# Kernel tuning notes

Hardware: AMD Instinct MI355X
Metric: run time of the kernel (lower is better)

The kernel has to match this reference:

```python
import jax, jax.numpy as jnp
import numpy as np

D = 1024
HEADS = 16
HEAD_DIM = D // HEADS
B = 4
L = 1024


def setup_inputs() -> dict:
    key = jax.random.key(0)
    kq, kk, kv, kw, kb = jax.random.split(key, 5)
    Q = jax.random.normal(kq, (B, L, D), dtype=jnp.float32)
    K = jax.random.normal(kk, (B, L, D), dtype=jnp.float32)
    V = jax.random.normal(kv, (B, L, D), dtype=jnp.float32)
    # Output projection H: torch nn.Linear(D, D) -> weight (D, D), bias (D,)
    lim = 1.0 / np.sqrt(D)
    W_H = jax.random.uniform(kw, (D, D), minval=-lim, maxval=lim, dtype=jnp.float32)
    b_H = jax.random.uniform(kb, (D,), minval=-lim, maxval=lim, dtype=jnp.float32)
    mask = 0  # falsy -> no masking branch, matching `if mask` in the source
    return {"Q": Q, "K": K, "V": V, "W_H": W_H, "b_H": b_H, "mask": mask}


def reference(Q, K, V, W_H, b_H, mask):
    batch, q_len, _ = Q.shape
    k_len = K.shape[1]
    Qh = Q.reshape(batch, q_len, HEADS, HEAD_DIM)
    Kh = K.reshape(batch, k_len, HEADS, HEAD_DIM)
    Vh = V.reshape(batch, k_len, HEADS, HEAD_DIM)
    scores = jnp.einsum('bqhd,bkhd->bhqk', Qh, Kh)  # [B,H,Lq,Lk]
    if mask:  # mask is a Python scalar (0 -> skip), as in source
        scores = jnp.where(mask == 0, -jnp.inf, scores)
    # NOTE: source scales by sqrt(D), not sqrt(head_dim)
    attn = jax.nn.softmax(scores / np.sqrt(D).astype(np.float32), axis=3)
    out = jnp.einsum('bhql,blhd->bqhd', attn, Vh).reshape(batch, q_len, D)
    return out @ W_H.T + b_H
```

## Files before the change

kernel.cpp:

```cpp
#include <hip/hip_runtime.h>
#include <hip/hip_bf16.h>

typedef __attribute__((ext_vector_type(4))) float f32x4;
typedef __attribute__((ext_vector_type(8))) short bf16x8;

constexpr int Bn  = 4;
constexpr int Ln  = 1024;
constexpr int Dn  = 1024;
constexpr int Hn  = 16;
constexpr int HDn = 64;

static __device__ __forceinline__ unsigned short bf16r(float f) {
    union { float f; unsigned int u; } x;
    x.f = f;
    unsigned int r = x.u + 0x7fffu + ((x.u >> 16) & 1u);
    return (unsigned short)(r >> 16);
}

__global__ __launch_bounds__(256) void cvt_kernel(
    const float* __restrict__ src, unsigned short* __restrict__ dst, int n4)
{
    int i = blockIdx.x * 256 + threadIdx.x;
    if (i < n4) {
        float4 v = ((const float4*)src)[i];
        ushort4 o;
        o.x = bf16r(v.x); o.y = bf16r(v.y); o.z = bf16r(v.z); o.w = bf16r(v.w);
        ((ushort4*)dst)[i] = o;
    }
}

__global__ __launch_bounds__(256) void vt_prep_kernel(
    const float* __restrict__ Vg, unsigned short* __restrict__ Vtg)
{
    __shared__ unsigned short T[64][72];
    const int tid = threadIdx.x;
    const int k0  = blockIdx.x * 64;
    const int h   = blockIdx.y;
    const int b   = blockIdx.z;
    const float* Vb = Vg + (size_t)b * Ln * Dn + h * HDn;

    for (int i = 0; i < 4; ++i) {
        int e4 = i * 256 + tid;
        int r = e4 >> 4, c4 = e4 & 15;
        float4 v = *(const float4*)(Vb + (size_t)(k0 + r) * Dn + c4 * 4);
        T[c4 * 4 + 0][r] = bf16r(v.x);
        T[c4 * 4 + 1][r] = bf16r(v.y);
        T[c4 * 4 + 2][r] = bf16r(v.z);
        T[c4 * 4 + 3][r] = bf16r(v.w);
    }
    __syncthreads();
    unsigned short* out = Vtg + ((size_t)(b * Hn + h) * HDn) * Ln + k0;
    for (int i = 0; i < 2; ++i) {
        int e8 = i * 256 + tid;
        int r = e8 >> 3, c8 = e8 & 7;
        *(uint4*)(out + (size_t)r * Ln + c8 * 8) = *(const uint4*)&T[r][c8 * 8];
    }
}

__global__ __launch_bounds__(256) void attn_kernel(
    const float* __restrict__ Qg, const unsigned short* __restrict__ Kbf,
    const unsigned short* __restrict__ Vtg, unsigned short* __restrict__ Xg)
{
    __shared__ unsigned short Ks[64][72];
    __shared__ unsigned short Vts[64][72];
    __shared__ unsigned short Ps[64][72];

    const int tid  = threadIdx.x;
    const int wave = tid >> 6;
    const int lane = tid & 63;
    const int l16  = lane & 15;
    const int quad = lane >> 4;

    const int q0 = blockIdx.x * 64;
    const int h  = blockIdx.y;
    const int b  = blockIdx.z;

    const unsigned short* Kb16 = Kbf + (size_t)b * Ln * Dn + h * HDn;
    const unsigned short* Vtb  = Vtg + ((size_t)(b * Hn + h) * HDn) * Ln;

    bf16x8 aq0, aq1;
    {
        const float* qp = Qg + ((size_t)b * Ln + q0 + wave * 16 + l16) * Dn
                             + h * HDn + quad * 8;
        float4 a0 = *(const float4*)qp;
        float4 a1 = *(const float4*)(qp + 4);
        float4 a2 = *(const float4*)(qp + 32);
        float4 a3 = *(const float4*)(qp + 36);
        aq0[0] = (short)bf16r(a0.x); aq0[1] = (short)bf16r(a0.y);
        aq0[2] = (short)bf16r(a0.z); aq0[3] = (short)bf16r(a0.w);
        aq0[4] = (short)bf16r(a1.x); aq0[5] = (short)bf16r(a1.y);
        aq0[6] = (short)bf16r(a1.z); aq0[7] = (short)bf16r(a1.w);
        aq1[0] = (short)bf16r(a2.x); aq1[1] = (short)bf16r(a2.y);
        aq1[2] = (short)bf16r(a2.z); aq1[3] = (short)bf16r(a2.w);
        aq1[4] = (short)bf16r(a3.x); aq1[5] = (short)bf16r(a3.y);
        aq1[6] = (short)bf16r(a3.z); aq1[7] = (short)bf16r(a3.w);
    }

    const float C = 0.04508422851562500f * 1.001553337f;
    const float SC = 1.4426950408889634f / 32.0f;
    (void)C;

    float lsum[4] = {0.f, 0.f, 0.f, 0.f};
    f32x4 Oacc[4];
    for (int d = 0; d < 4; ++d) Oacc[d] = (f32x4){0.f, 0.f, 0.f, 0.f};

    for (int it = 0; it < Ln / 64; ++it) {
        const int k0 = it * 64;
        __syncthreads();
        {
            int r = tid >> 3, c8 = tid & 7;
            const unsigned short* kp = Kb16 + (size_t)(k0 + r) * Dn + c8 * 8;
            *(uint4*)&Ks[r][c8 * 8]      = *(const uint4*)kp;
            *(uint4*)&Ks[r + 32][c8 * 8] = *(const uint4*)(kp + (size_t)32 * Dn);
            const unsigned short* vp = Vtb + (size_t)r * Ln + k0 + c8 * 8;
            *(uint4*)&Vts[r][c8 * 8]      = *(const uint4*)vp;
            *(uint4*)&Vts[r + 32][c8 * 8] = *(const uint4*)(vp + (size_t)32 * Ln);
        }
        __syncthreads();

        f32x4 s[4];
        for (int n = 0; n < 4; ++n) {
            bf16x8 b0 = *(const bf16x8*)&Ks[n * 16 + l16][quad * 8];
            bf16x8 b1 = *(const bf16x8*)&Ks[n * 16 + l16][32 + quad * 8];
            f32x4 acc = (f32x4){0.f, 0.f, 0.f, 0.f};
            acc = __builtin_amdgcn_mfma_f32_16x16x32_bf16(aq0, b0, acc, 0, 0, 0);
            acc = __builtin_amdgcn_mfma_f32_16x16x32_bf16(aq1, b1, acc, 0, 0, 0);
            s[n] = acc;
        }

        for (int n = 0; n < 4; ++n)
            for (int r = 0; r < 4; ++r) {
                float p = exp2f(s[n][r] * SC);
                s[n][r] = p;
                lsum[r] += p;
            }

        for (int n = 0; n < 4; ++n)
            for (int r = 0; r < 4; ++r)
                Ps[wave * 16 + quad * 4 + r][n * 16 + l16] = bf16r(s[n][r]);

        for (int kk = 0; kk < 2; ++kk) {
            bf16x8 ap = *(const bf16x8*)&Ps[wave * 16 + l16][kk * 32 + quad * 8];
            for (int d = 0; d < 4; ++d) {
                bf16x8 bv = *(const bf16x8*)&Vts[d * 16 + l16][kk * 32 + quad * 8];
                Oacc[d] = __builtin_amdgcn_mfma_f32_16x16x32_bf16(ap, bv, Oacc[d], 0, 0, 0);
            }
        }
    }

    float linv[4];
    for (int r = 0; r < 4; ++r) {
        float rs = lsum[r];
        rs += __shfl_xor(rs, 1, 64);
        rs += __shfl_xor(rs, 2, 64);
        rs += __shfl_xor(rs, 4, 64);
        rs += __shfl_xor(rs, 8, 64);
        linv[r] = 1.f / rs;
    }

    unsigned short* Xb = Xg + ((size_t)b * Ln + q0) * Dn + h * HDn;
    for (int r = 0; r < 4; ++r) {
        int row = wave * 16 + quad * 4 + r;
        for (int d = 0; d < 4; ++d)
            Xb[(size_t)row * Dn + d * 16 + l16] = bf16r(Oacc[d][r] * linv[r]);
    }
}

__global__ __launch_bounds__(512) void proj_kernel(
    const unsigned short* __restrict__ Xg, const unsigned short* __restrict__ Wbf,
    const float* __restrict__ bg, float* __restrict__ Yg)
{
    __shared__ unsigned short Xs[128][72];
    __shared__ unsigned short Wsh[128][72];

    const int tid  = threadIdx.x;
    const int wave = tid >> 6;
    const int lane = tid & 63;
    const int l16  = lane & 15;
    const int quad = lane >> 4;
    const int mw   = (wave & 1) * 64;
    const int nw   = (wave >> 1) * 32;

    const int m0 = blockIdx.x * 128;
    const int n0 = blockIdx.y * 128;

    f32x4 acc[4][2];
    for (int mt = 0; mt < 4; ++mt)
        for (int nt = 0; nt < 2; ++nt)
            acc[mt][nt] = (f32x4){0.f, 0.f, 0.f, 0.f};

    for (int it = 0; it < Dn / 64; ++it) {
        const int kk0 = it * 64;
        __syncthreads();
        {
            int r = tid >> 3, c8 = tid & 7;
            const unsigned short* xp = Xg + (size_t)(m0 + r) * Dn + kk0 + c8 * 8;
            *(uint4*)&Xs[r][c8 * 8]      = *(const uint4*)xp;
            *(uint4*)&Xs[r + 64][c8 * 8] = *(const uint4*)(xp + (size_t)64 * Dn);
            const unsigned short* wp = Wbf + (size_t)(n0 + r) * Dn + kk0 + c8 * 8;
            *(uint4*)&Wsh[r][c8 * 8]      = *(const uint4*)wp;
            *(uint4*)&Wsh[r + 64][c8 * 8] = *(const uint4*)(wp + (size_t)64 * Dn);
        }
        __syncthreads();

        bf16x8 af[4][2], bfr[2][2];
        for (int mt = 0; mt < 4; ++mt)
            for (int kk = 0; kk < 2; ++kk)
                af[mt][kk] = *(const bf16x8*)&Xs[mw + mt * 16 + l16][kk * 32 + quad * 8];
        for (int nt = 0; nt < 2; ++nt)
            for (int kk = 0; kk < 2; ++kk)
                bfr[nt][kk] = *(const bf16x8*)&Wsh[nw + nt * 16 + l16][kk * 32 + quad * 8];
        for (int mt = 0; mt < 4; ++mt)
            for (int nt = 0; nt < 2; ++nt) {
                acc[mt][nt] = __builtin_amdgcn_mfma_f32_16x16x32_bf16(
                    af[mt][0], bfr[nt][0], acc[mt][nt], 0, 0, 0);
                acc[mt][nt] = __builtin_amdgcn_mfma_f32_16x16x32_bf16(
                    af[mt][1], bfr[nt][1], acc[mt][nt], 0, 0, 0);
            }
    }

    for (int nt = 0; nt < 2; ++nt) {
        int col = n0 + nw + nt * 16 + l16;
        float bb = bg[col];
        for (int mt = 0; mt < 4; ++mt)
            for (int r = 0; r < 4; ++r) {
                int row = m0 + mw + mt * 16 + quad * 4 + r;
                Yg[(size_t)row * Dn + col] = acc[mt][nt][r] + bb;
            }
    }
}

extern "C" void kernel_launch(void* const* d_in, const int* in_sizes, int n_in,
                              void* d_out, int out_size, void* d_ws, size_t ws_size,
                              hipStream_t stream) {
    const float* Q    = (const float*)d_in[0];
    const float* K    = (const float*)d_in[1];
    const float* V    = (const float*)d_in[2];
    const float* W    = (const float*)d_in[3];
    const float* bias = (const float*)d_in[4];

    unsigned short* Kbf = (unsigned short*)d_ws;
    unsigned short* Vt  = Kbf + (size_t)Bn * Ln * Dn;
    unsigned short* Wbf = Vt  + (size_t)Bn * Ln * Dn;
    unsigned short* X   = Wbf + (size_t)Dn * Dn;
    float* Y = (float*)d_out;

    cvt_kernel<<<(Bn * Ln * Dn / 4 + 255) / 256, 256, 0, stream>>>(K, Kbf, Bn * Ln * Dn / 4);
    cvt_kernel<<<(Dn * Dn / 4 + 255) / 256, 256, 0, stream>>>(W, Wbf, Dn * Dn / 4);

    dim3 gv(Ln / 64, Hn, Bn);
    vt_prep_kernel<<<gv, 256, 0, stream>>>(V, Vt);

    dim3 g1(Ln / 64, Hn, Bn);
    attn_kernel<<<g1, 256, 0, stream>>>(Q, Kbf, Vt, X);

    dim3 g2((Bn * Ln) / 128, Dn / 128);
    proj_kernel<<<g2, 512, 0, stream>>>(X, Wbf, bias, Y);
}
```

Baseline: 166.3 us.

## Fuse K/V/W conversion kernels, widen attention blocks, retile projection GEMM

Merges the K and W bf16 conversion and the V transpose into one prep kernel, which removes two launches and shares the index math. The attention kernel moves to 512 threads and 128 query rows per block, so each K/V tile loaded into shared memory serves twice as many queries. The projection GEMM switches to 64x64 tiles with a K-step of 128 and 256 threads, which gives more blocks and fewer barriers. The trade-offs are lower per-block reuse in the GEMM and a longer dependency chain in the larger attention blocks.

Result: faster. 155.9 us (-6.2%).

```diff
diff --git a/kernel.cpp b/kernel.cpp
--- a/kernel.cpp
+++ b/kernel.cpp
@@ -17,36 +17,46 @@
     return (unsigned short)(r >> 16);
 }
 
-__global__ __launch_bounds__(256) void cvt_kernel(
-    const float* __restrict__ src, unsigned short* __restrict__ dst, int n4)
+__global__ __launch_bounds__(256) void prep_kernel(
+    const float* __restrict__ Kg, const float* __restrict__ Vg,
+    const float* __restrict__ Wg, unsigned short* __restrict__ Kbf,
+    unsigned short* __restrict__ Vtg, unsigned short* __restrict__ Wbf)
 {
-    int i = blockIdx.x * 256 + threadIdx.x;
-    if (i < n4) {
-        float4 v = ((const float4*)src)[i];
-        ushort4 o;
-        o.x = bf16r(v.x); o.y = bf16r(v.y); o.z = bf16r(v.z); o.w = bf16r(v.w);
-        ((ushort4*)dst)[i] = o;
-    }
-}
-
-__global__ __launch_bounds__(256) void vt_prep_kernel(
-    const float* __restrict__ Vg, unsigned short* __restrict__ Vtg)
-{
+    const int tid = threadIdx.x;
+    if (blockIdx.z == 4) {
+        const int r0 = blockIdx.x * 64, c0 = blockIdx.y * 64;
+        for (int i = 0; i < 4; ++i) {
+            int e4 = i * 256 + tid;
+            int r = e4 >> 4, c4 = e4 & 15;
+            const float* p = Wg + (size_t)(r0 + r) * Dn + c0 + c4 * 4;
+            float4 v = *(const float4*)p;
+            ushort4 o;
+            o.x = bf16r(v.x); o.y = bf16r(v.y); o.z = bf16r(v.z); o.w = bf16r(v.w);
+            *(ushort4*)(Wbf + (size_t)(r0 + r) * Dn + c0 + c4 * 4) = o;
+        }
+        return;
+    }
+
     __shared__ unsigned short T[64][72];
-    const int tid = threadIdx.x;
-    const int k0  = blockIdx.x * 64;
-    const int h   = blockIdx.y;
-    const int b   = blockIdx.z;
+    const int k0 = blockIdx.x * 64;
+    const int h  = blockIdx.y;
+    const int b  = blockIdx.z;
+    const float* Kb = Kg + (size_t)b * Ln * Dn + h * HDn;
     const float* Vb = Vg + (size_t)b * Ln * Dn + h * HDn;
+    unsigned short* Ko = Kbf + (size_t)b * Ln * Dn + h * HDn;
 
     for (int i = 0; i < 4; ++i) {
         int e4 = i * 256 + tid;
         int r = e4 >> 4, c4 = e4 & 15;
-        float4 v = *(const float4*)(Vb + (size_t)(k0 + r) * Dn + c4 * 4);
-        T[c4 * 4 + 0][r] = bf16r(v.x);
-        T[c4 * 4 + 1][r] = bf16r(v.y);
-        T[c4 * 4 + 2][r] = bf16r(v.z);
-        T[c4 * 4 + 3][r] = bf16r(v.w);
+        float4 kv = *(const float4*)(Kb + (size_t)(k0 + r) * Dn + c4 * 4);
+        ushort4 o;
+        o.x = bf16r(kv.x); o.y = bf16r(kv.y); o.z = bf16r(kv.z); o.w = bf16r(kv.w);
+        *(ushort4*)(Ko + (size_t)(k0 + r) * Dn + c4 * 4) = o;
+        float4 vv = *(const float4*)(Vb + (size_t)(k0 + r) * Dn + c4 * 4);
+        T[c4 * 4 + 0][r] = bf16r(vv.x);
+        T[c4 * 4 + 1][r] = bf16r(vv.y);
+        T[c4 * 4 + 2][r] = bf16r(vv.z);
+        T[c4 * 4 + 3][r] = bf16r(vv.w);
     }
     __syncthreads();
     unsigned short* out = Vtg + ((size_t)(b * Hn + h) * HDn) * Ln + k0;
@@ -57,13 +67,13 @@
     }
 }
 
-__global__ __launch_bounds__(256) void attn_kernel(
+__global__ __launch_bounds__(512) void attn_kernel(
     const float* __restrict__ Qg, const unsigned short* __restrict__ Kbf,
     const unsigned short* __restrict__ Vtg, unsigned short* __restrict__ Xg)
 {
     __shared__ unsigned short Ks[64][72];
     __shared__ unsigned short Vts[64][72];
-    __shared__ unsigned short Ps[64][72];
+    __shared__ unsigned short Ps[128][72];
 
     const int tid  = threadIdx.x;
     const int wave = tid >> 6;
@@ -71,7 +81,7 @@
     const int l16  = lane & 15;
     const int quad = lane >> 4;
 
-    const int q0 = blockIdx.x * 64;
+    const int q0 = blockIdx.x * 128;
     const int h  = blockIdx.y;
     const int b  = blockIdx.z;
 
@@ -96,9 +106,7 @@
         aq1[6] = (short)bf16r(a3.z); aq1[7] = (short)bf16r(a3.w);
     }
 
-    const float C = 0.04508422851562500f * 1.001553337f;
     const float SC = 1.4426950408889634f / 32.0f;
-    (void)C;
 
     float lsum[4] = {0.f, 0.f, 0.f, 0.f};
     f32x4 Oacc[4];
@@ -109,12 +117,10 @@
         __syncthreads();
         {
             int r = tid >> 3, c8 = tid & 7;
-            const unsigned short* kp = Kb16 + (size_t)(k0 + r) * Dn + c8 * 8;
-            *(uint4*)&Ks[r][c8 * 8]      = *(const uint4*)kp;
-            *(uint4*)&Ks[r + 32][c8 * 8] = *(const uint4*)(kp + (size_t)32 * Dn);
-            const unsigned short* vp = Vtb + (size_t)r * Ln + k0 + c8 * 8;
-            *(uint4*)&Vts[r][c8 * 8]      = *(const uint4*)vp;
-            *(uint4*)&Vts[r + 32][c8 * 8] = *(const uint4*)(vp + (size_t)32 * Ln);
+            *(uint4*)&Ks[r][c8 * 8] =
+                *(const uint4*)(Kb16 + (size_t)(k0 + r) * Dn + c8 * 8);
+            *(uint4*)&Vts[r][c8 * 8] =
+                *(const uint4*)(Vtb + (size_t)r * Ln + k0 + c8 * 8);
         }
         __syncthreads();
 
@@ -166,63 +172,59 @@
     }
 }
 
-__global__ __launch_bounds__(512) void proj_kernel(
+__global__ __launch_bounds__(256) void proj_kernel(
     const unsigned short* __restrict__ Xg, const unsigned short* __restrict__ Wbf,
     const float* __restrict__ bg, float* __restrict__ Yg)
 {
-    __shared__ unsigned short Xs[128][72];
-    __shared__ unsigned short Wsh[128][72];
+    __shared__ unsigned short Xs[64][136];
+    __shared__ unsigned short Wsh[64][136];
 
     const int tid  = threadIdx.x;
     const int wave = tid >> 6;
     const int lane = tid & 63;
     const int l16  = lane & 15;
     const int quad = lane >> 4;
-    const int mw   = (wave & 1) * 64;
+    const int mw   = (wave & 1) * 32;
     const int nw   = (wave >> 1) * 32;
 
-    const int m0 = blockIdx.x * 128;
-    const int n0 = blockIdx.y * 128;
-
-    f32x4 acc[4][2];
-    for (int mt = 0; mt < 4; ++mt)
+    const int m0 = blockIdx.x * 64;
+    const int n0 = blockIdx.y * 64;
+
+    f32x4 acc[2][2];
+    for (int mt = 0; mt < 2; ++mt)
         for (int nt = 0; nt < 2; ++nt)
             acc[mt][nt] = (f32x4){0.f, 0.f, 0.f, 0.f};
 
-    for (int it = 0; it < Dn / 64; ++it) {
-        const int kk0 = it * 64;
-        __syncthreads();
-        {
-            int r = tid >> 3, c8 = tid & 7;
-            const unsigned short* xp = Xg + (size_t)(m0 + r) * Dn + kk0 + c8 * 8;
-            *(uint4*)&Xs[r][c8 * 8]      = *(const uint4*)xp;
-            *(uint4*)&Xs[r + 64][c8 * 8] = *(const uint4*)(xp + (size_t)64 * Dn);
-            const unsigned short* wp = Wbf + (size_t)(n0 + r) * Dn + kk0 + c8 * 8;
-            *(uint4*)&Wsh[r][c8 * 8]      = *(const uint4*)wp;
-            *(uint4*)&Wsh[r + 64][c8 * 8] = *(const uint4*)(wp + (size_t)64 * Dn);
-        }
-        __syncthreads();
-
-        bf16x8 af[4][2], bfr[2][2];
-        for (int mt = 0; mt < 4; ++mt)
-            for (int kk = 0; kk < 2; ++kk)
-                af[mt][kk] = *(const bf16x8*)&Xs[mw + mt * 16 + l16][kk * 32 + quad * 8];
-        for (int nt = 0; nt < 2; ++nt)
-            for (int kk = 0; kk < 2; ++kk)
-                bfr[nt][kk] = *(const bf16x8*)&Wsh[nw + nt * 16 + l16][kk * 32 + quad * 8];
-        for (int mt = 0; mt < 4; ++mt)
-            for (int nt = 0; nt < 2; ++nt) {
-                acc[mt][nt] = __builtin_amdgcn_mfma_f32_16x16x32_bf16(
-                    af[mt][0], bfr[nt][0], acc[mt][nt], 0, 0, 0);
-                acc[mt][nt] = __builtin_amdgcn_mfma_f32_16x16x32_bf16(
-                    af[mt][1], bfr[nt][1], acc[mt][nt], 0, 0, 0);
-            }
+    for (int it = 0; it < Dn / 128; ++it) {
+        const int kk0 = it * 128;
+        __syncthreads();
+        for (int i = 0; i < 4; ++i) {
+            int idx = i * 256 + tid;
+            int r = idx >> 4, c8 = idx & 15;
+            *(uint4*)&Xs[r][c8 * 8] =
+                *(const uint4*)(Xg + (size_t)(m0 + r) * Dn + kk0 + c8 * 8);
+            *(uint4*)&Wsh[r][c8 * 8] =
+                *(const uint4*)(Wbf + (size_t)(n0 + r) * Dn + kk0 + c8 * 8);
+        }
+        __syncthreads();
+
+        for (int kk = 0; kk < 4; ++kk) {
+            bf16x8 af[2], bfr[2];
+            for (int mt = 0; mt < 2; ++mt)
+                af[mt] = *(const bf16x8*)&Xs[mw + mt * 16 + l16][kk * 32 + quad * 8];
+            for (int nt = 0; nt < 2; ++nt)
+                bfr[nt] = *(const bf16x8*)&Wsh[nw + nt * 16 + l16][kk * 32 + quad * 8];
+            for (int mt = 0; mt < 2; ++mt)
+                for (int nt = 0; nt < 2; ++nt)
+                    acc[mt][nt] = __builtin_amdgcn_mfma_f32_16x16x32_bf16(
+                        af[mt], bfr[nt], acc[mt][nt], 0, 0, 0);
+        }
     }
 
     for (int nt = 0; nt < 2; ++nt) {
         int col = n0 + nw + nt * 16 + l16;
         float bb = bg[col];
-        for (int mt = 0; mt < 4; ++mt)
+        for (int mt = 0; mt < 2; ++mt)
             for (int r = 0; r < 4; ++r) {
                 int row = m0 + mw + mt * 16 + quad * 4 + r;
                 Yg[(size_t)row * Dn + col] = acc[mt][nt][r] + bb;
@@ -245,15 +247,12 @@
     unsigned short* X   = Wbf + (size_t)Dn * Dn;
     float* Y = (float*)d_out;
 
-    cvt_kernel<<<(Bn * Ln * Dn / 4 + 255) / 256, 256, 0, stream>>>(K, Kbf, Bn * Ln * Dn / 4);
-    cvt_kernel<<<(Dn * Dn / 4 + 255) / 256, 256, 0, stream>>>(W, Wbf, Dn * Dn / 4);
-
-    dim3 gv(Ln / 64, Hn, Bn);
-    vt_prep_kernel<<<gv, 256, 0, stream>>>(V, Vt);
-
-    dim3 g1(Ln / 64, Hn, Bn);
-    attn_kernel<<<g1, 256, 0, stream>>>(Q, Kbf, Vt, X);
-
-    dim3 g2((Bn * Ln) / 128, Dn / 128);
-    proj_kernel<<<g2, 512, 0, stream>>>(X, Wbf, bias, Y);
-}
+    dim3 gp(Ln / 64, Hn, Bn + 1);
+    prep_kernel<<<gp, 256, 0, stream>>>(K, V, W, Kbf, Vt, Wbf);
+
+    dim3 g1(Ln / 128, Hn, Bn);
+    attn_kernel<<<g1, 512, 0, stream>>>(Q, Kbf, Vt, X);
+
+    dim3 g2((Bn * Ln) / 64, Dn / 64);
+    proj_kernel<<<g2, 256, 0, stream>>>(X, Wbf, bias, Y);
+}
```
